# Kernel tuning notes

Hardware: AMD Instinct MI355X
Metric: run time of the kernel (lower is better)

## Reference

```python
import jax, jax.numpy as jnp
import numpy as np

EPS = 1e-5
NUM_GROUPS = 8


def group_norm(x, gamma, beta):
    # x: [B, C, T]; normalize per group over (C/G, T)
    B, C, T = x.shape
    G = NUM_GROUPS
    xg = x.reshape(B, G, C // G, T)
    mean = xg.mean(axis=(2, 3), keepdims=True)
    var = xg.var(axis=(2, 3), keepdims=True)
    xn = ((xg - mean) * jax.lax.rsqrt(var + EPS)).reshape(B, C, T)
    return xn * gamma[None, :, None] + beta[None, :, None]


def mish(x):
    return x * jnp.tanh(jax.nn.softplus(x))


def setup_inputs() -> dict:
    key = jax.random.key(0)
    ks = jax.random.split(key, 7)
    C, Cb, B, T = 1024, 256, 64, 512
    # conv1d kernel_size=1 weights stored as [out, in]
    w_down = jax.random.normal(ks[0], (Cb, C), dtype=jnp.float32) / np.sqrt(C)
    b_down = jax.random.normal(ks[1], (Cb,), dtype=jnp.float32) * 0.01
    w_up = jax.random.normal(ks[2], (C, Cb), dtype=jnp.float32) / np.sqrt(Cb)
    b_up = jax.random.normal(ks[3], (C,), dtype=jnp.float32) * 0.01
    gamma = jnp.ones((C,), dtype=jnp.float32)
    beta = jnp.zeros((C,), dtype=jnp.float32)
    x = jax.random.normal(ks[4], (B, C, T), dtype=jnp.float32)
    return {"x": x, "gamma": gamma, "beta": beta,
            "w_down": w_down, "b_down": b_down,
            "w_up": w_up, "b_up": b_up}


def reference(x, gamma, beta, w_down, b_down, w_up, b_up):
    residual = x
    h = group_norm(x, gamma, beta)                       # [B, C, T]
    h = jnp.einsum('bct,oc->bot', h, w_down) + b_down[None, :, None]  # [B, Cb, T]
    h = mish(h)
    h = jnp.einsum('bct,oc->bot', h, w_up) + b_up[None, :, None]      # [B, C, T]
    return h + residual
```

## Files before the change

### kernel.cpp

```cpp
#include <hip/hip_runtime.h>
#include <hip/hip_bf16.h>
#include <stddef.h>

#define B_   64
#define C_   1024
#define CB_  256
#define T_   512
#define G_   8
#define N_   32768
#define EPS_ 1e-5f

using short8  = __attribute__((ext_vector_type(8))) short;
using short4v = __attribute__((ext_vector_type(4))) short;
using f32x4   = __attribute__((ext_vector_type(4))) float;

__device__ __forceinline__ short f2bf(float f) {
    unsigned u = __float_as_uint(f);
    u += 0x7fffu + ((u >> 16) & 1u);
    return (short)(u >> 16);
}

__device__ __forceinline__ float mish_f(float y) {
    float u = __expf(fminf(y, 30.f));
    float w = u * u + 2.f * u;
    return y * (w / (w + 2.f));
}

__global__ void prep_weights(const float* __restrict__ wd, const float* __restrict__ wu,
                             short* __restrict__ wdb, short* __restrict__ wut) {
    int i = blockIdx.x * 256 + threadIdx.x;
    if (i < CB_ * C_) {
        wdb[i] = f2bf(wd[i]);
        int m = i >> 8, k = i & 255;
        int idx = (((m >> 4) * 8 + (k >> 5)) << 9) + (((k >> 3) & 3) << 7)
                + ((m & 15) << 3) + (k & 7);
        wut[idx] = f2bf(wu[i]);
    }
}

__global__ void stats_kernel(const float* __restrict__ x, const float* __restrict__ gamma,
                             const float* __restrict__ beta,
                             float* __restrict__ scaleW, float* __restrict__ shiftW) {
    const int tid = threadIdx.x;
    const int bg = blockIdx.x;
    const int b = bg >> 3, g = bg & 7;
    const float4* p = (const float4*)(x + ((size_t)b * C_ + g * 128) * T_);
    float s = 0.f, q = 0.f;
    for (int i = tid; i < 16384; i += 256) {
        float4 v = p[i];
        s += v.x + v.y + v.z + v.w;
        q += v.x * v.x + v.y * v.y + v.z * v.z + v.w * v.w;
    }
    for (int o = 32; o > 0; o >>= 1) {
        s += __shfl_down(s, o);
        q += __shfl_down(q, o);
    }
    __shared__ float red[8];
    __shared__ float mr[2];
    const int wid = tid >> 6, lane = tid & 63;
    if (lane == 0) { red[wid] = s; red[4 + wid] = q; }
    __syncthreads();
    if (tid == 0) {
        float S = red[0] + red[1] + red[2] + red[3];
        float Q = red[4] + red[5] + red[6] + red[7];
        float mean = S * (1.f / 65536.f);
        float var = Q * (1.f / 65536.f) - mean * mean;
        mr[0] = mean;
        mr[1] = rsqrtf(var + EPS_);
    }
    __syncthreads();
    float mean = mr[0], rstd = mr[1];
    if (tid < 128) {
        int c = g * 128 + tid;
        float sc = rstd * gamma[c];
        scaleW[b * C_ + c] = sc;
        shiftW[b * C_ + c] = beta[c] - mean * sc;
    }
}

#define LDSTR 40
#define MSTR  264

#define BAR() { asm volatile("s_waitcnt lgkmcnt(0)" ::: "memory"); __builtin_amdgcn_s_barrier(); }

__global__ __launch_bounds__(512, 2) void fused_adapter(
    const float* __restrict__ x, const short* __restrict__ wd,
    const float* __restrict__ b_down,
    const float* __restrict__ scaleW, const float* __restrict__ shiftW,
    const short* __restrict__ wut, const float* __restrict__ b_up,
    float* __restrict__ out) {
    __shared__ short As0[256 * LDSTR];
    __shared__ short As1[256 * LDSTR];
    __shared__ short Bs0[128 * LDSTR];
    __shared__ short Bs1[128 * LDSTR];
    __shared__ float sS[C_], sT[C_];
    __shared__ short Ms[128 * MSTR];

    const int tid = threadIdx.x;
    const int n0 = blockIdx.x * 128;
    const int b  = n0 >> 9;
    const int t0 = n0 & 511;

    for (int i = tid; i < C_; i += 512) {
        sS[i] = scaleW[b * C_ + i];
        sT[i] = shiftW[b * C_ + i];
    }

    const int a_kc = tid & 3;
    const int a_m  = tid >> 2;
    const int b_n  = tid & 127;
    const int b_kg = tid >> 7;
    const int wid  = tid >> 6;
    const int lane = tid & 63;
    const int wm = wid >> 1, wn = wid & 1;
    const int q = lane >> 4, l16 = lane & 15;

    f32x4 acc[4][4];
#pragma unroll
    for (int i = 0; i < 4; i++)
#pragma unroll
        for (int j = 0; j < 4; j++) acc[i][j] = 0.f;

    const float* xb = x + (size_t)b * C_ * T_ + t0;

#define ISSUE(kt, aa0, aa1, bb) { \
    const short* src = wd + a_m * C_ + (kt) * 32 + a_kc * 8; \
    aa0 = *(const short8*)src; \
    aa1 = *(const short8*)(src + 128 * C_); \
    const float* xp = xb + (size_t)((kt) * 32 + b_kg * 8) * T_ + b_n; \
    _Pragma("unroll") for (int i_ = 0; i_ < 8; i_++) bb[i_] = xp[(size_t)i_ * T_]; }

#define STORE(kt, As_, Bs_, aa0, aa1, bb) { \
    *(short8*)&As_[a_m * LDSTR + a_kc * 8] = aa0; \
    *(short8*)&As_[(a_m + 128) * LDSTR + a_kc * 8] = aa1; \
    const int kb_ = (kt) * 32 + b_kg * 8; \
    short8 v_; \
    _Pragma("unroll") for (int i_ = 0; i_ < 8; i_++) v_[i_] = f2bf(bb[i_] * sS[kb_ + i_] + sT[kb_ + i_]); \
    *(short8*)&Bs_[b_n * LDSTR + b_kg * 8] = v_; }

#define MFMA_STEP(As_, Bs_) { \
    short8 af_[4], bf_[4]; \
    _Pragma("unroll") for (int i_ = 0; i_ < 4; i_++) \
        af_[i_] = *(const short8*)&As_[(wm * 64 + i_ * 16 + l16) * LDSTR + q * 8]; \
    _Pragma("unroll") for (int j_ = 0; j_ < 4; j_++) \
        bf_[j_] = *(const short8*)&Bs_[(wn * 64 + j_ * 16 + l16) * LDSTR + q * 8]; \
    _Pragma("unroll") for (int i_ = 0; i_ < 4; i_++) \
    _Pragma("unroll") for (int j_ = 0; j_ < 4; j_++) \
        acc[i_][j_] = __builtin_amdgcn_mfma_f32_16x16x32_bf16(af_[i_], bf_[j_], acc[i_][j_], 0, 0, 0); }

    short8 a0A, a1A, a0B, a1B;
    float bvA[8], bvB[8];
    ISSUE(0, a0A, a1A, bvA);
    ISSUE(1, a0B, a1B, bvB);
    BAR();
    STORE(0, As0, Bs0, a0A, a1A, bvA);
    BAR();

#pragma unroll 1
    for (int kt2 = 0; kt2 < 16; ++kt2) {
        const int kt = kt2 * 2;
        if (kt + 2 < 32) ISSUE(kt + 2, a0A, a1A, bvA);
        MFMA_STEP(As0, Bs0);
        STORE(kt + 1, As1, Bs1, a0B, a1B, bvB);
        BAR();
        if (kt + 3 < 32) ISSUE(kt + 3, a0B, a1B, bvB);
        MFMA_STEP(As1, Bs1);
        if (kt + 2 < 32) STORE(kt + 2, As0, Bs0, a0A, a1A, bvA);
        BAR();
    }

#pragma unroll
    for (int i = 0; i < 4; i++) {
        const int o_b = wm * 64 + i * 16 + q * 4;
        const float bd0 = b_down[o_b];
        const float bd1 = b_down[o_b + 1];
        const float bd2 = b_down[o_b + 2];
        const float bd3 = b_down[o_b + 3];
#pragma unroll
        for (int j = 0; j < 4; j++) {
            const int nl = wn * 64 + j * 16 + l16;
            short4v v;
            v[0] = f2bf(mish_f(acc[i][j][0] + bd0));
            v[1] = f2bf(mish_f(acc[i][j][1] + bd1));
            v[2] = f2bf(mish_f(acc[i][j][2] + bd2));
            v[3] = f2bf(mish_f(acc[i][j][3] + bd3));
            *(short4v*)&Ms[nl * MSTR + o_b] = v;
        }
    }
    BAR();

#pragma unroll 1
    for (int half = 0; half < 2; ++half) {
        f32x4 a2[4][8];
#pragma unroll
        for (int i = 0; i < 4; i++)
#pragma unroll
            for (int j = 0; j < 8; j++) a2[i][j] = 0.f;

        const int mbb = half * 32 + wid * 4;
#pragma unroll 2
        for (int kt = 0; kt < 8; ++kt) {
            short8 af[4], bf2[8];
#pragma unroll
            for (int i = 0; i < 4; i++)
                af[i] = *(const short8*)(wut + ((size_t)((mbb + i) * 8 + kt) << 9) + lane * 8);
#pragma unroll
            for (int j = 0; j < 8; j++)
                bf2[j] = *(const short8*)&Ms[(j * 16 + l16) * MSTR + kt * 32 + q * 8];
#pragma unroll
            for (int i = 0; i < 4; i++)
#pragma unroll
                for (int j = 0; j < 8; j++)
                    a2[i][j] = __builtin_amdgcn_mfma_f32_16x16x32_bf16(af[i], bf2[j], a2[i][j], 0, 0, 0);
        }

#pragma unroll
        for (int i = 0; i < 4; i++) {
            const int c_b = half * 512 + wid * 64 + i * 16 + q * 4;
            const float bu0 = b_up[c_b];
            const float bu1 = b_up[c_b + 1];
            const float bu2 = b_up[c_b + 2];
            const float bu3 = b_up[c_b + 3];
#pragma unroll
            for (int j = 0; j < 8; j++) {
                const int tt = t0 + j * 16 + l16;
                const size_t gi = ((size_t)b * C_ + c_b) * T_ + tt;
                out[gi]              = a2[i][j][0] + bu0 + x[gi];
                out[gi + T_]         = a2[i][j][1] + bu1 + x[gi + T_];
                out[gi + 2 * T_]     = a2[i][j][2] + bu2 + x[gi + 2 * T_];
                out[gi + 3 * T_]     = a2[i][j][3] + bu3 + x[gi + 3 * T_];
            }
        }
    }
#undef ISSUE
#undef STORE
#undef MFMA_STEP
}

extern "C" void kernel_launch(void* const* d_in, const int* in_sizes, int n_in,
                              void* d_out, int out_size, void* d_ws, size_t ws_size,
                              hipStream_t stream) {
    const float* x      = (const float*)d_in[0];
    const float* gamma  = (const float*)d_in[1];
    const float* beta   = (const float*)d_in[2];
    const float* w_down = (const float*)d_in[3];
    const float* b_down = (const float*)d_in[4];
    const float* w_up   = (const float*)d_in[5];
    const float* b_up   = (const float*)d_in[6];
    float* out = (float*)d_out;

    float* scaleW = (float*)d_ws;
    float* shiftW = scaleW + B_ * C_;
    short* wdb    = (short*)(shiftW + B_ * C_);
    short* wut    = wdb + CB_ * C_;

    prep_weights<<<dim3((CB_ * C_ + 255) / 256), 256, 0, stream>>>(w_down, w_up, wdb, wut);
    stats_kernel<<<dim3(B_ * G_), 256, 0, stream>>>(x, gamma, beta, scaleW, shiftW);
    fused_adapter<<<dim3(N_ / 128), 512, 0, stream>>>(x, wdb, b_down, scaleW, shiftW,
                                                      wut, b_up, out);
}
```

Before: 320.0 us.

## Pre-normalize x to bf16 in stats pass and load down-weights as pre-swizzled fragments

The stats kernel now makes a second pass over each group and writes the normalized activations as a bf16 tensor, so the fused GEMM kernel reads half-width data with no per-element scale/shift. The down-projection weights are pre-swizzled into MFMA fragment order and loaded straight from global memory into registers, which removes the A-tile LDS staging and shrinks shared memory use. The cost is an extra read of x and a 64 MB bf16 write plus read through the workspace, and the weight fragment loads now go directly to global/L2 each k-step.

```diff
diff --git a/kernel.cpp b/kernel.cpp
--- a/kernel.cpp
+++ b/kernel.cpp
@@ -27,24 +27,31 @@
 }
 
 __global__ void prep_weights(const float* __restrict__ wd, const float* __restrict__ wu,
-                             short* __restrict__ wdb, short* __restrict__ wut) {
+                             short* __restrict__ wdt, short* __restrict__ wut) {
     int i = blockIdx.x * 256 + threadIdx.x;
     if (i < CB_ * C_) {
-        wdb[i] = f2bf(wd[i]);
-        int m = i >> 8, k = i & 255;
-        int idx = (((m >> 4) * 8 + (k >> 5)) << 9) + (((k >> 3) & 3) << 7)
-                + ((m & 15) << 3) + (k & 7);
-        wut[idx] = f2bf(wu[i]);
+        {
+            int m = i >> 10, k = i & 1023;
+            int idx = (((m >> 4) * 32 + (k >> 5)) << 9) + (((k >> 3) & 3) << 7)
+                    + ((m & 15) << 3) + (k & 7);
+            wdt[idx] = f2bf(wd[i]);
+        }
+        {
+            int m = i >> 8, k = i & 255;
+            int idx = (((m >> 4) * 8 + (k >> 5)) << 9) + (((k >> 3) & 3) << 7)
+                    + ((m & 15) << 3) + (k & 7);
+            wut[idx] = f2bf(wu[i]);
+        }
     }
 }
 
 __global__ void stats_kernel(const float* __restrict__ x, const float* __restrict__ gamma,
-                             const float* __restrict__ beta,
-                             float* __restrict__ scaleW, float* __restrict__ shiftW) {
+                             const float* __restrict__ beta, short* __restrict__ xh) {
     const int tid = threadIdx.x;
     const int bg = blockIdx.x;
     const int b = bg >> 3, g = bg & 7;
-    const float4* p = (const float4*)(x + ((size_t)b * C_ + g * 128) * T_);
+    const size_t base = ((size_t)b * C_ + g * 128) * T_;
+    const float4* p = (const float4*)(x + base);
     float s = 0.f, q = 0.f;
     for (int i = tid; i < 16384; i += 256) {
         float4 v = p[i];
@@ -57,6 +64,7 @@
     }
     __shared__ float red[8];
     __shared__ float mr[2];
+    __shared__ float sls[128], slt[128];
     const int wid = tid >> 6, lane = tid & 63;
     if (lane == 0) { red[wid] = s; red[4 + wid] = q; }
     __syncthreads();
@@ -69,12 +77,24 @@
         mr[1] = rsqrtf(var + EPS_);
     }
     __syncthreads();
-    float mean = mr[0], rstd = mr[1];
     if (tid < 128) {
         int c = g * 128 + tid;
-        float sc = rstd * gamma[c];
-        scaleW[b * C_ + c] = sc;
-        shiftW[b * C_ + c] = beta[c] - mean * sc;
+        float sc = mr[1] * gamma[c];
+        sls[tid] = sc;
+        slt[tid] = beta[c] - mr[0] * sc;
+    }
+    __syncthreads();
+    short4v* xq = (short4v*)(xh + base);
+    for (int i = tid; i < 16384; i += 256) {
+        float4 v = p[i];
+        const int cl = i >> 7;
+        const float sc = sls[cl], sh = slt[cl];
+        short4v o;
+        o[0] = f2bf(v.x * sc + sh);
+        o[1] = f2bf(v.y * sc + sh);
+        o[2] = f2bf(v.z * sc + sh);
+        o[3] = f2bf(v.w * sc + sh);
+        xq[i] = o;
     }
 }
 
@@ -84,16 +104,12 @@
 #define BAR() { asm volatile("s_waitcnt lgkmcnt(0)" ::: "memory"); __builtin_amdgcn_s_barrier(); }
 
 __global__ __launch_bounds__(512, 2) void fused_adapter(
-    const float* __restrict__ x, const short* __restrict__ wd,
-    const float* __restrict__ b_down,
-    const float* __restrict__ scaleW, const float* __restrict__ shiftW,
+    const short* __restrict__ xh, const float* __restrict__ x,
+    const short* __restrict__ wdt, const float* __restrict__ b_down,
     const short* __restrict__ wut, const float* __restrict__ b_up,
     float* __restrict__ out) {
-    __shared__ short As0[256 * LDSTR];
-    __shared__ short As1[256 * LDSTR];
     __shared__ short Bs0[128 * LDSTR];
     __shared__ short Bs1[128 * LDSTR];
-    __shared__ float sS[C_], sT[C_];
     __shared__ short Ms[128 * MSTR];
 
     const int tid = threadIdx.x;
@@ -101,13 +117,6 @@
     const int b  = n0 >> 9;
     const int t0 = n0 & 511;
 
-    for (int i = tid; i < C_; i += 512) {
-        sS[i] = scaleW[b * C_ + i];
-        sT[i] = shiftW[b * C_ + i];
-    }
-
-    const int a_kc = tid & 3;
-    const int a_m  = tid >> 2;
     const int b_n  = tid & 127;
     const int b_kg = tid >> 7;
     const int wid  = tid >> 6;
@@ -121,51 +130,50 @@
 #pragma unroll
         for (int j = 0; j < 4; j++) acc[i][j] = 0.f;
 
-    const float* xb = x + (size_t)b * C_ * T_ + t0;
-
-#define ISSUE(kt, aa0, aa1, bb) { \
-    const short* src = wd + a_m * C_ + (kt) * 32 + a_kc * 8; \
-    aa0 = *(const short8*)src; \
-    aa1 = *(const short8*)(src + 128 * C_); \
-    const float* xp = xb + (size_t)((kt) * 32 + b_kg * 8) * T_ + b_n; \
+    const unsigned short* xhb = (const unsigned short*)xh + (size_t)b * C_ * T_ + t0;
+
+#define ISSUE_B(kt, bb) { \
+    const unsigned short* xp = xhb + (size_t)((kt) * 32 + b_kg * 8) * T_ + b_n; \
     _Pragma("unroll") for (int i_ = 0; i_ < 8; i_++) bb[i_] = xp[(size_t)i_ * T_]; }
 
-#define STORE(kt, As_, Bs_, aa0, aa1, bb) { \
-    *(short8*)&As_[a_m * LDSTR + a_kc * 8] = aa0; \
-    *(short8*)&As_[(a_m + 128) * LDSTR + a_kc * 8] = aa1; \
-    const int kb_ = (kt) * 32 + b_kg * 8; \
+#define STORE_B(Bs_, bb) { \
     short8 v_; \
-    _Pragma("unroll") for (int i_ = 0; i_ < 8; i_++) v_[i_] = f2bf(bb[i_] * sS[kb_ + i_] + sT[kb_ + i_]); \
+    _Pragma("unroll") for (int i_ = 0; i_ < 8; i_++) v_[i_] = (short)bb[i_]; \
     *(short8*)&Bs_[b_n * LDSTR + b_kg * 8] = v_; }
 
-#define MFMA_STEP(As_, Bs_) { \
-    short8 af_[4], bf_[4]; \
+#define AFRAG(kt, ff) { \
     _Pragma("unroll") for (int i_ = 0; i_ < 4; i_++) \
-        af_[i_] = *(const short8*)&As_[(wm * 64 + i_ * 16 + l16) * LDSTR + q * 8]; \
+        ff[i_] = *(const short8*)(wdt + ((size_t)((wm * 4 + i_) * 32 + (kt)) << 9) + lane * 8); }
+
+#define MFMA_STEP(Bs_, ff) { \
+    short8 bf_[4]; \
     _Pragma("unroll") for (int j_ = 0; j_ < 4; j_++) \
         bf_[j_] = *(const short8*)&Bs_[(wn * 64 + j_ * 16 + l16) * LDSTR + q * 8]; \
     _Pragma("unroll") for (int i_ = 0; i_ < 4; i_++) \
     _Pragma("unroll") for (int j_ = 0; j_ < 4; j_++) \
-        acc[i_][j_] = __builtin_amdgcn_mfma_f32_16x16x32_bf16(af_[i_], bf_[j_], acc[i_][j_], 0, 0, 0); }
-
-    short8 a0A, a1A, a0B, a1B;
-    float bvA[8], bvB[8];
-    ISSUE(0, a0A, a1A, bvA);
-    ISSUE(1, a0B, a1B, bvB);
-    BAR();
-    STORE(0, As0, Bs0, a0A, a1A, bvA);
+        acc[i_][j_] = __builtin_amdgcn_mfma_f32_16x16x32_bf16(ff[i_], bf_[j_], acc[i_][j_], 0, 0, 0); }
+
+    unsigned short bvA[8], bvB[8];
+    short8 fA[4], fB[4];
+    AFRAG(0, fA);
+    ISSUE_B(0, bvA);
+    ISSUE_B(1, bvB);
+    AFRAG(1, fB);
+    STORE_B(Bs0, bvA);
     BAR();
 
 #pragma unroll 1
     for (int kt2 = 0; kt2 < 16; ++kt2) {
         const int kt = kt2 * 2;
-        if (kt + 2 < 32) ISSUE(kt + 2, a0A, a1A, bvA);
-        MFMA_STEP(As0, Bs0);
-        STORE(kt + 1, As1, Bs1, a0B, a1B, bvB);
+        if (kt + 2 < 32) ISSUE_B(kt + 2, bvA);
+        MFMA_STEP(Bs0, fA);
+        if (kt + 2 < 32) AFRAG(kt + 2, fA);
+        STORE_B(Bs1, bvB);
         BAR();
-        if (kt + 3 < 32) ISSUE(kt + 3, a0B, a1B, bvB);
-        MFMA_STEP(As1, Bs1);
-        if (kt + 2 < 32) STORE(kt + 2, As0, Bs0, a0A, a1A, bvA);
+        if (kt + 3 < 32) ISSUE_B(kt + 3, bvB);
+        MFMA_STEP(Bs1, fB);
+        if (kt + 3 < 32) AFRAG(kt + 3, fB);
+        if (kt + 2 < 32) STORE_B(Bs0, bvA);
         BAR();
     }
 
@@ -232,8 +240,9 @@
             }
         }
     }
-#undef ISSUE
-#undef STORE
+#undef ISSUE_B
+#undef STORE_B
+#undef AFRAG
 #undef MFMA_STEP
 }
 
@@ -249,13 +258,11 @@
     const float* b_up   = (const float*)d_in[6];
     float* out = (float*)d_out;
 
-    float* scaleW = (float*)d_ws;
-    float* shiftW = scaleW + B_ * C_;
-    short* wdb    = (short*)(shiftW + B_ * C_);
-    short* wut    = wdb + CB_ * C_;
-
-    prep_weights<<<dim3((CB_ * C_ + 255) / 256), 256, 0, stream>>>(w_down, w_up, wdb, wut);
-    stats_kernel<<<dim3(B_ * G_), 256, 0, stream>>>(x, gamma, beta, scaleW, shiftW);
-    fused_adapter<<<dim3(N_ / 128), 512, 0, stream>>>(x, wdb, b_down, scaleW, shiftW,
-                                                      wut, b_up, out);
-}
+    short* xh  = (short*)d_ws;
+    short* wdt = xh + (size_t)B_ * C_ * T_;
+    short* wut = wdt + CB_ * C_;
+
+    prep_weights<<<dim3((CB_ * C_ + 255) / 256), 256, 0, stream>>>(w_down, w_up, wdt, wut);
+    stats_kernel<<<dim3(B_ * G_), 256, 0, stream>>>(x, gamma, beta, xh);
+    fused_adapter<<<dim3(N_ / 128), 512, 0, stream>>>(xh, x, wdt, b_down, wut, b_up, out);
+}
```

Measured after the change: 360.4 us. +12.6%, slower.
